# Performance work log

Hardware: AMD Instinct MI355X
Metric: run time of the kernel (lower is better)

## Reference

```python
import jax, jax.numpy as jnp
import numpy as np

N = 100000   # nodes
E = 1600000  # edges
R = 8        # relations
B = 8        # bases (min(R, hidden))
IN = 128; HID = 128; OUT = 128
BN_EPS = 1e-5


def setup_inputs() -> dict:
    key = jax.random.key(0)
    ks = jax.random.split(key, 20)
    s = 0.1  # xavier-ish small gain as in reset_parameters
    f32 = jnp.float32
    inp = {
        'x': jax.random.normal(ks[0], (N, IN), f32),
        'edge_index': jax.random.randint(ks[1], (2, E), 0, N, dtype=jnp.int32),
        'edge_type': jax.random.randint(ks[2], (E,), 0, R, dtype=jnp.int32),
        # RGCNConv layer 1 (basis decomposition)
        'basis1': jax.random.normal(ks[3], (B, IN, HID), f32) * s,
        'comp1': jax.random.normal(ks[4], (R, B), f32) * s,
        'root1': jax.random.normal(ks[5], (IN, HID), f32) * s,
        'bias1': jnp.zeros((HID,), f32),
        # layer 2
        'basis2': jax.random.normal(ks[6], (B, HID, HID), f32) * s,
        'comp2': jax.random.normal(ks[7], (R, B), f32) * s,
        'root2': jax.random.normal(ks[8], (HID, HID), f32) * s,
        'bias2': jnp.zeros((HID,), f32),
        # layer 3
        'basis3': jax.random.normal(ks[9], (B, HID, OUT), f32) * s,
        'comp3': jax.random.normal(ks[10], (R, B), f32) * s,
        'root3': jax.random.normal(ks[11], (HID, OUT), f32) * s,
        'bias3': jnp.zeros((OUT,), f32),
        # BatchNorm affine params (batch-stat normalization)
        'bn1_gamma': jnp.ones((HID,), f32),
        'bn1_beta': jnp.zeros((HID,), f32),
        'bn2_gamma': jnp.ones((HID,), f32),
        'bn2_beta': jnp.zeros((HID,), f32),
    }
    return inp


def rgcn_conv(x, basis, comp, root, bias, src, dst, etype):
    # relation weights from basis decomposition: W[r] = sum_b comp[r,b] * basis[b]
    W = jnp.einsum('rb,bio->rio', comp, basis)  # [R, in, out]
    # mean aggregation per (dst, relation); transform after mean (linearity)
    seg = dst.astype(jnp.int32) * R + etype.astype(jnp.int32)  # [E]
    msg_sum = jax.ops.segment_sum(x[src], seg, num_segments=N * R)  # [N*R, in]
    cnt = jax.ops.segment_sum(jnp.ones((src.shape[0],), x.dtype), seg, num_segments=N * R)
    mean = msg_sum / jnp.maximum(cnt, 1.0)[:, None]
    mean = mean.reshape(N, R, -1)  # [N, R, in]
    out = jnp.einsum('nri,rio->no', mean, W) + x @ root + bias
    return out


def batchnorm(h, gamma, beta):
    m = h.mean(axis=0)
    v = h.var(axis=0)
    return (h - m) * jax.lax.rsqrt(v + BN_EPS) * gamma + beta


def reference(x, edge_index, edge_type,
              basis1, comp1, root1, bias1,
              basis2, comp2, root2, bias2,
              basis3, comp3, root3, bias3,
              bn1_gamma, bn1_beta, bn2_gamma, bn2_beta):
    src, dst = edge_index[0], edge_index[1]
    h = rgcn_conv(x, basis1, comp1, root1, bias1, src, dst, edge_type)
    h = batchnorm(h, bn1_gamma, bn1_beta)
    h = jnp.where(h > 0, h, 0.1 * h)  # LeakyReLU(0.1); dropout inactive (eval)
    h = rgcn_conv(h, basis2, comp2, root2, bias2, src, dst, edge_type)
    h = batchnorm(h, bn2_gamma, bn2_beta)
    h = jnp.where(h > 0, h, 0.1 * h)
    h = rgcn_conv(h, basis3, comp3, root3, bias3, src, dst, edge_type)
    # F.normalize(p=2, dim=1)
    norm = jnp.maximum(jnp.sqrt(jnp.sum(h * h, axis=1, keepdims=True)), 1e-12)
    return h / norm
```

## Files before the change

### kernel.cpp

```cpp
#include <hip/hip_runtime.h>

#define NN 100000
#define EE 1600000
#define RRR 8
#define NSEG (NN*RRR)
#define F 128
#define KDIM 1152
#define NKT 36
#define BNEPS 1e-5f

typedef __attribute__((ext_vector_type(8))) short bf16x8;
typedef __attribute__((ext_vector_type(8))) unsigned short u16x8;
typedef __attribute__((ext_vector_type(4))) float f32x4;

static __device__ __forceinline__ unsigned short bf16r(float f) {
  unsigned u = __float_as_uint(f);
  u += 0x7fffu + ((u >> 16) & 1u);
  return (unsigned short)(u >> 16);
}
static __device__ __forceinline__ float b2f(unsigned short s) {
  return __uint_as_float((unsigned)s << 16);
}

__global__ void k_count(const int* __restrict__ dst, const int* __restrict__ et,
                        unsigned* __restrict__ cnt) {
  int e = blockIdx.x*256 + threadIdx.x;
  if (e < EE) {
    int seg = dst[e]*RRR + et[e];
    atomicAdd(&cnt[seg], 1u);
  }
}

__global__ void k_scan1(const unsigned* __restrict__ cnt, unsigned* __restrict__ off,
                        unsigned* __restrict__ bsum) {
  __shared__ unsigned s[256];
  int t = threadIdx.x;
  int base = blockIdx.x*2048 + t*8;
  unsigned loc[8];
  unsigned tot = 0;
#pragma unroll
  for (int j = 0; j < 8; j++) {
    unsigned v = (base+j < NSEG) ? cnt[base+j] : 0u;
    loc[j] = tot;
    tot += v;
  }
  s[t] = tot;
  __syncthreads();
  for (int d = 1; d < 256; d <<= 1) {
    unsigned v = (t >= d) ? s[t-d] : 0u;
    __syncthreads();
    s[t] += v;
    __syncthreads();
  }
  unsigned tbase = s[t] - tot;
#pragma unroll
  for (int j = 0; j < 8; j++)
    if (base+j < NSEG) off[base+j] = tbase + loc[j];
  if (t == 255) bsum[blockIdx.x] = s[255];
}

__global__ void k_scan2(unsigned* bsum, int nb) {
  __shared__ unsigned s[512];
  int t = threadIdx.x;
  unsigned v = (t < nb) ? bsum[t] : 0u;
  s[t] = v;
  __syncthreads();
  for (int d = 1; d < 512; d <<= 1) {
    unsigned u = (t >= d) ? s[t-d] : 0u;
    __syncthreads();
    s[t] += u;
    __syncthreads();
  }
  if (t < nb) bsum[t] = (t == 0) ? 0u : s[t-1];
}

__global__ void k_scan3(unsigned* off, const unsigned* __restrict__ bsum) {
  int i = blockIdx.x*256 + threadIdx.x;
  if (i < NSEG) off[i] += bsum[i >> 11];
}

__global__ void k_fill(const int* __restrict__ src, const int* __restrict__ dst,
                       const int* __restrict__ et, const unsigned* __restrict__ off,
                       unsigned* __restrict__ fillc, int* __restrict__ csr) {
  int e = blockIdx.x*256 + threadIdx.x;
  if (e < EE) {
    int seg = dst[e]*RRR + et[e];
    unsigned pos = off[seg] + atomicAdd(&fillc[seg], 1u);
    csr[pos] = src[e];
  }
}

__global__ void k_cvt(const float* __restrict__ x, unsigned short* __restrict__ xb) {
  int i = blockIdx.x*256 + threadIdx.x;
  if (i < NN*32) {
    float4 v = ((const float4*)x)[i];
    ushort4 o;
    o.x = bf16r(v.x); o.y = bf16r(v.y); o.z = bf16r(v.z); o.w = bf16r(v.w);
    ((ushort4*)xb)[i] = o;
  }
}

__global__ void k_makeW(const float* __restrict__ basis, const float* __restrict__ comp,
                        const float* __restrict__ root, unsigned short* __restrict__ WB) {
  int kt = blockIdx.x;
  int ct = blockIdx.y;
  int lane = threadIdx.x;
  int o = ct*16 + (lane & 15);
  int kbase = kt*32 + (lane >> 4)*8;
  unsigned short v[8];
#pragma unroll
  for (int j = 0; j < 8; j++) {
    int k = kbase + j;
    float val;
    if (k < 1024) {
      int r = k >> 7, i = k & 127;
      val = 0.f;
#pragma unroll
      for (int b = 0; b < 8; b++)
        val += comp[r*8+b] * basis[(b*F + i)*F + o];
    } else {
      val = root[(k - 1024)*F + o];
    }
    v[j] = bf16r(val);
  }
  unsigned short* dst = WB + ((size_t)(kt*8 + ct)*64 + lane)*8;
#pragma unroll
  for (int j = 0; j < 8; j++) dst[j] = v[j];
}

__global__ __launch_bounds__(256) void k_agg(const unsigned short* __restrict__ hb,
    const unsigned* __restrict__ off, const unsigned* __restrict__ cnt,
    const int* __restrict__ csr, unsigned short* __restrict__ Mean,
    int base, int count) {
  int t = threadIdx.x;
  int sl = t & 15;
  int c8 = sl * 8;
  int sidx = t >> 4;
  int nl = sidx >> 3;
  int r  = sidx & 7;
  int nloc = blockIdx.x*2 + nl;
  if (nloc > count-1) nloc = count-1;
  int node = base + nloc;
  int seg = node*RRR + r;
  unsigned b0 = off[seg];
  unsigned k = cnt[seg];
  float a[8];
#pragma unroll
  for (int u = 0; u < 8; u++) a[u] = 0.f;
  unsigned j = 0;
  for (; j + 2 <= k; j += 2) {
    int iA = csr[b0+j];
    int iB = csr[b0+j+1];
    u16x8 va = *(const u16x8*)&hb[(size_t)iA*F + c8];
    u16x8 vb = *(const u16x8*)&hb[(size_t)iB*F + c8];
#pragma unroll
    for (int u = 0; u < 8; u++) a[u] += b2f(va[u]) + b2f(vb[u]);
  }
  if (j < k) {
    int iA = csr[b0+j];
    u16x8 va = *(const u16x8*)&hb[(size_t)iA*F + c8];
#pragma unroll
    for (int u = 0; u < 8; u++) a[u] += b2f(va[u]);
  }
  float inv = k ? 1.f/(float)k : 0.f;
  u16x8 o;
#pragma unroll
  for (int u = 0; u < 8; u++) o[u] = bf16r(a[u]*inv);
  size_t mrow = (size_t)nloc * KDIM;
  *(u16x8*)&Mean[mrow + r*F + c8] = o;
  if (r == 0)
    *(u16x8*)&Mean[mrow + 1024 + c8] = *(const u16x8*)&hb[(size_t)node*F + c8];
}

__global__ __launch_bounds__(256) void k_gemm(const unsigned short* __restrict__ Mean,
    const unsigned short* __restrict__ WB, const float* __restrict__ bias,
    float* __restrict__ outp, float* __restrict__ stats,
    int outBase, int count, int mode) {
  __shared__ float s_sum[128];
  __shared__ float s_sq[128];
  int t = threadIdx.x;
  int wave = t >> 6;
  int lane = t & 63;
  int rbase = blockIdx.x*128 + wave*32;
  int rlo = lane & 15;
  int kg = lane >> 4;
  int r0 = rbase + rlo;       if (r0 > count-1) r0 = count-1;
  int r1 = rbase + 16 + rlo;  if (r1 > count-1) r1 = count-1;
  const unsigned short* a0p = Mean + (size_t)r0*KDIM + kg*8;
  const unsigned short* a1p = Mean + (size_t)r1*KDIM + kg*8;
  const unsigned short* bp  = WB + (size_t)lane*8;

  if (mode == 0 && t < 128) { s_sum[t] = 0.f; s_sq[t] = 0.f; }

  f32x4 acc[2][8];
#pragma unroll
  for (int i = 0; i < 2; i++)
#pragma unroll
    for (int j = 0; j < 8; j++) acc[i][j] = (f32x4){0.f,0.f,0.f,0.f};

  for (int kt = 0; kt < NKT; kt++) {
    bf16x8 a0 = *(const bf16x8*)(a0p + kt*32);
    bf16x8 a1 = *(const bf16x8*)(a1p + kt*32);
#pragma unroll
    for (int ct = 0; ct < 8; ct++) {
      bf16x8 b = *(const bf16x8*)(bp + (size_t)(kt*8 + ct)*64*8);
      acc[0][ct] = __builtin_amdgcn_mfma_f32_16x16x32_bf16(a0, b, acc[0][ct], 0, 0, 0);
      acc[1][ct] = __builtin_amdgcn_mfma_f32_16x16x32_bf16(a1, b, acc[1][ct], 0, 0, 0);
    }
  }

  float bv[8];
#pragma unroll
  for (int ct = 0; ct < 8; ct++) bv[ct] = bias[ct*16 + rlo];

  if (mode == 0) {
    __syncthreads();
    float psum[8], psq[8];
#pragma unroll
    for (int ct = 0; ct < 8; ct++) { psum[ct] = 0.f; psq[ct] = 0.f; }
#pragma unroll
    for (int rt = 0; rt < 2; rt++) {
#pragma unroll
      for (int i = 0; i < 4; i++) {
        int row = rbase + rt*16 + kg*4 + i;
        if (row < count) {
          float* orow = outp + (size_t)(outBase + row)*F;
#pragma unroll
          for (int ct = 0; ct < 8; ct++) {
            float y = acc[rt][ct][i] + bv[ct];
            orow[ct*16 + rlo] = y;
            psum[ct] += y;
            psq[ct]  += y*y;
          }
        }
      }
    }
#pragma unroll
    for (int ct = 0; ct < 8; ct++) {
      atomicAdd(&s_sum[ct*16 + rlo], psum[ct]);
      atomicAdd(&s_sq [ct*16 + rlo], psq[ct]);
    }
    __syncthreads();
    if (t < 128) {
      atomicAdd(&stats[t],       s_sum[t]);
      atomicAdd(&stats[128 + t], s_sq[t]);
    }
  } else {
#pragma unroll
    for (int rt = 0; rt < 2; rt++) {
#pragma unroll
      for (int i = 0; i < 4; i++) {
        int row = rbase + rt*16 + kg*4 + i;
        float y[8];
        float ss = 0.f;
#pragma unroll
        for (int ct = 0; ct < 8; ct++) {
          y[ct] = acc[rt][ct][i] + bv[ct];
          ss += y[ct]*y[ct];
        }
#pragma unroll
        for (int m = 1; m < 16; m <<= 1)
          ss += __shfl_xor(ss, m, 64);
        float inv = 1.f / fmaxf(sqrtf(ss), 1e-12f);
        if (row < count) {
          float* orow = outp + (size_t)(outBase + row)*F;
#pragma unroll
          for (int ct = 0; ct < 8; ct++)
            orow[ct*16 + rlo] = y[ct]*inv;
        }
      }
    }
  }
}

__global__ __launch_bounds__(256) void k_bnapply(const float* __restrict__ h,
    const float* __restrict__ stats, const float* __restrict__ gamma,
    const float* __restrict__ beta, unsigned short* __restrict__ outp) {
  int idx = blockIdx.x*256 + threadIdx.x;
  if (idx >= NN*32) return;
  int row = idx >> 5;
  int c4 = (idx & 31) * 4;
  float4 v  = *(const float4*)&h[(size_t)row*F + c4];
  float4 sm = *(const float4*)&stats[c4];
  float4 sq = *(const float4*)&stats[128 + c4];
  float4 g  = *(const float4*)&gamma[c4];
  float4 bt = *(const float4*)&beta[c4];
  const float invN = 1.f / (float)NN;
  ushort4 o;
  { float m = sm.x*invN; float var = sq.x*invN - m*m; float r0 = rsqrtf(var + BNEPS);
    float z = (v.x - m)*r0*g.x + bt.x; o.x = bf16r((z > 0.f) ? z : 0.1f*z); }
  { float m = sm.y*invN; float var = sq.y*invN - m*m; float r0 = rsqrtf(var + BNEPS);
    float z = (v.y - m)*r0*g.y + bt.y; o.y = bf16r((z > 0.f) ? z : 0.1f*z); }
  { float m = sm.z*invN; float var = sq.z*invN - m*m; float r0 = rsqrtf(var + BNEPS);
    float z = (v.z - m)*r0*g.z + bt.z; o.z = bf16r((z > 0.f) ? z : 0.1f*z); }
  { float m = sm.w*invN; float var = sq.w*invN - m*m; float r0 = rsqrtf(var + BNEPS);
    float z = (v.w - m)*r0*g.w + bt.w; o.w = bf16r((z > 0.f) ? z : 0.1f*z); }
  *(ushort4*)&outp[(size_t)row*F + c4] = o;
}

extern "C" void kernel_launch(void* const* d_in, const int* in_sizes, int n_in,
                              void* d_out, int out_size, void* d_ws, size_t ws_size,
                              hipStream_t stream) {
  const float* x      = (const float*)d_in[0];
  const int*   ei     = (const int*)d_in[1];
  const int*   etp    = (const int*)d_in[2];
  const float* basis[3] = {(const float*)d_in[3], (const float*)d_in[7],  (const float*)d_in[11]};
  const float* comp[3]  = {(const float*)d_in[4], (const float*)d_in[8],  (const float*)d_in[12]};
  const float* root[3]  = {(const float*)d_in[5], (const float*)d_in[9],  (const float*)d_in[13]};
  const float* bias[3]  = {(const float*)d_in[6], (const float*)d_in[10], (const float*)d_in[14]};
  const float* gamma[2] = {(const float*)d_in[15], (const float*)d_in[17]};
  const float* beta[2]  = {(const float*)d_in[16], (const float*)d_in[18]};
  const int* srcv = ei;
  const int* dstv = ei + EE;
  float* out = (float*)d_out;

  char* w = (char*)d_ws;
  size_t p = 0;
  auto take = [&](size_t bytes) -> void* {
    void* q = w + p;
    p = (p + bytes + 255) & ~(size_t)255;
    return q;
  };
  unsigned* cnt   = (unsigned*)take((size_t)NSEG*4);
  unsigned* off   = (unsigned*)take((size_t)NSEG*4);
  unsigned* fillc = (unsigned*)take((size_t)NSEG*4);
  int*      csr   = (int*)     take((size_t)EE*4);
  unsigned* bsum  = (unsigned*)take(1024*4);
  unsigned short* WB = (unsigned short*)take((size_t)KDIM*F*2);
  float*    stats = (float*)   take(256*4);
  float*    wsA   = (float*)   take((size_t)NN*F*4);
  unsigned short* wsBb = (unsigned short*)take((size_t)NN*F*2);
  unsigned short* xb   = (unsigned short*)take((size_t)NN*F*2);
  size_t avail = (ws_size > p) ? (ws_size - p) : 0;
  long long chmax = (long long)(avail / ((size_t)KDIM*2));
  int CH = (chmax > NN) ? NN : (int)chmax;
  if (CH < 2) CH = 2;
  unsigned short* Mean = (unsigned short*)(w + p);

  hipMemsetAsync(cnt,   0, (size_t)NSEG*4, stream);
  hipMemsetAsync(fillc, 0, (size_t)NSEG*4, stream);
  k_count<<<(EE+255)/256, 256, 0, stream>>>(dstv, etp, cnt);
  int nb1 = (NSEG + 2047)/2048;
  k_scan1<<<nb1, 256, 0, stream>>>(cnt, off, bsum);
  k_scan2<<<1, 512, 0, stream>>>(bsum, nb1);
  k_scan3<<<(NSEG+255)/256, 256, 0, stream>>>(off, bsum);
  k_fill<<<(EE+255)/256, 256, 0, stream>>>(srcv, dstv, etp, off, fillc, csr);
  k_cvt<<<(NN*32+255)/256, 256, 0, stream>>>(x, xb);

  for (int l = 0; l < 3; l++) {
    const unsigned short* hin = (l == 0) ? xb : wsBb;
    float* hraw = (l == 2) ? out : wsA;
    int mode = (l == 2) ? 1 : 0;
    dim3 gw(NKT, 8);
    k_makeW<<<gw, 64, 0, stream>>>(basis[l], comp[l], root[l], WB);
    if (l < 2) hipMemsetAsync(stats, 0, 256*4, stream);
    for (int b0n = 0; b0n < NN; b0n += CH) {
      int cc = NN - b0n; if (cc > CH) cc = CH;
      k_agg<<<(cc+1)/2, 256, 0, stream>>>(hin, off, cnt, csr, Mean, b0n, cc);
      k_gemm<<<(cc+127)/128, 256, 0, stream>>>(Mean, WB, bias[l], hraw, stats, b0n, cc, mode);
    }
    if (l < 2)
      k_bnapply<<<(NN*32+255)/256, 256, 0, stream>>>(hraw, stats, gamma[l], beta[l], wsBb);
  }
}
```

Baseline: 897.9 us.

## Fuse aggregation into GEMM via LDS tiles and rebuild CSR with bucketed sort

The per-layer aggregation and GEMM kernels become one fused kernel. It builds each relation's mean (and the root slice) for 64 nodes into swizzled LDS, then feeds MFMA directly, so the large bf16 Mean buffer in global memory is no longer written and re-read. The CSR build is also replaced by a two-level bucket sort: a coarse histogram and scatter by destination block, then per-bucket local counting in LDS. This avoids global atomics over 800K segments and the multi-pass scan. In exchange, aggregation work is serialized per relation behind barriers inside each block, which can reduce latency hiding, and src is packed into 17 bits.

```diff
diff --git a/kernel.cpp b/kernel.cpp
--- a/kernel.cpp
+++ b/kernel.cpp
@@ -5,8 +5,8 @@
 #define RRR 8
 #define NSEG (NN*RRR)
 #define F 128
-#define KDIM 1152
-#define NKT 36
+#define NBK 196
+#define NT 64
 #define BNEPS 1e-5f
 
 typedef __attribute__((ext_vector_type(8))) short bf16x8;
@@ -21,72 +21,90 @@
 static __device__ __forceinline__ float b2f(unsigned short s) {
   return __uint_as_float((unsigned)s << 16);
 }
-
-__global__ void k_count(const int* __restrict__ dst, const int* __restrict__ et,
-                        unsigned* __restrict__ cnt) {
+static __device__ __forceinline__ int swz(int a) {
+  return a ^ (((a >> 8) & 7) << 4);
+}
+
+__global__ void k_hist(const int* __restrict__ dst, unsigned* __restrict__ bhist) {
+  __shared__ unsigned h[NBK];
+  int t = threadIdx.x;
+  if (t < NBK) h[t] = 0;
+  __syncthreads();
+  for (int e = blockIdx.x*256 + t; e < EE; e += gridDim.x*256)
+    atomicAdd(&h[((unsigned)dst[e]) >> 9], 1u);
+  __syncthreads();
+  if (t < NBK) atomicAdd(&bhist[t], h[t]);
+}
+
+__global__ void k_scanb(const unsigned* __restrict__ bhist, unsigned* __restrict__ boff) {
+  __shared__ unsigned s[256];
+  int t = threadIdx.x;
+  unsigned v = (t < NBK) ? bhist[t] : 0u;
+  s[t] = v;
+  __syncthreads();
+  for (int d = 1; d < 256; d <<= 1) {
+    unsigned u = (t >= d) ? s[t-d] : 0u;
+    __syncthreads();
+    s[t] += u;
+    __syncthreads();
+  }
+  if (t < NBK) boff[t] = s[t] - v;
+  if (t == NBK-1) boff[NBK] = s[t];
+}
+
+__global__ void k_scatter(const int* __restrict__ src, const int* __restrict__ dst,
+                          const int* __restrict__ et, const unsigned* __restrict__ boff,
+                          unsigned* __restrict__ bfill, unsigned* __restrict__ ebuf) {
   int e = blockIdx.x*256 + threadIdx.x;
   if (e < EE) {
-    int seg = dst[e]*RRR + et[e];
-    atomicAdd(&cnt[seg], 1u);
-  }
-}
-
-__global__ void k_scan1(const unsigned* __restrict__ cnt, unsigned* __restrict__ off,
-                        unsigned* __restrict__ bsum) {
-  __shared__ unsigned s[256];
-  int t = threadIdx.x;
-  int base = blockIdx.x*2048 + t*8;
-  unsigned loc[8];
-  unsigned tot = 0;
-#pragma unroll
-  for (int j = 0; j < 8; j++) {
-    unsigned v = (base+j < NSEG) ? cnt[base+j] : 0u;
-    loc[j] = tot;
-    tot += v;
-  }
-  s[t] = tot;
+    int d = dst[e];
+    int b = ((unsigned)d) >> 9;
+    unsigned pos = boff[b] + atomicAdd(&bfill[b], 1u);
+    ebuf[pos] = (((unsigned)((d & 511)*RRR + et[e])) << 17) | (unsigned)src[e];
+  }
+}
+
+__global__ __launch_bounds__(256) void k_bucket(const unsigned* __restrict__ boff,
+    const unsigned* __restrict__ ebuf, unsigned* __restrict__ off,
+    unsigned* __restrict__ cnt, int* __restrict__ csr) {
+  __shared__ unsigned lcnt[4096];
+  __shared__ unsigned loff[4096];
+  __shared__ unsigned wsum[256];
+  int b = blockIdx.x, t = threadIdx.x;
+  unsigned s0 = boff[b], e0 = boff[b+1];
+  for (int i = t; i < 4096; i += 256) lcnt[i] = 0;
+  __syncthreads();
+  for (unsigned i = s0 + t; i < e0; i += 256)
+    atomicAdd(&lcnt[ebuf[i] >> 17], 1u);
+  __syncthreads();
+  unsigned run = 0, tmp[16];
+  int base16 = t*16;
+#pragma unroll
+  for (int j = 0; j < 16; j++) { tmp[j] = run; run += lcnt[base16 + j]; }
+  wsum[t] = run;
   __syncthreads();
   for (int d = 1; d < 256; d <<= 1) {
-    unsigned v = (t >= d) ? s[t-d] : 0u;
-    __syncthreads();
-    s[t] += v;
-    __syncthreads();
-  }
-  unsigned tbase = s[t] - tot;
-#pragma unroll
-  for (int j = 0; j < 8; j++)
-    if (base+j < NSEG) off[base+j] = tbase + loc[j];
-  if (t == 255) bsum[blockIdx.x] = s[255];
-}
-
-__global__ void k_scan2(unsigned* bsum, int nb) {
-  __shared__ unsigned s[512];
-  int t = threadIdx.x;
-  unsigned v = (t < nb) ? bsum[t] : 0u;
-  s[t] = v;
-  __syncthreads();
-  for (int d = 1; d < 512; d <<= 1) {
-    unsigned u = (t >= d) ? s[t-d] : 0u;
-    __syncthreads();
-    s[t] += u;
-    __syncthreads();
-  }
-  if (t < nb) bsum[t] = (t == 0) ? 0u : s[t-1];
-}
-
-__global__ void k_scan3(unsigned* off, const unsigned* __restrict__ bsum) {
-  int i = blockIdx.x*256 + threadIdx.x;
-  if (i < NSEG) off[i] += bsum[i >> 11];
-}
-
-__global__ void k_fill(const int* __restrict__ src, const int* __restrict__ dst,
-                       const int* __restrict__ et, const unsigned* __restrict__ off,
-                       unsigned* __restrict__ fillc, int* __restrict__ csr) {
-  int e = blockIdx.x*256 + threadIdx.x;
-  if (e < EE) {
-    int seg = dst[e]*RRR + et[e];
-    unsigned pos = off[seg] + atomicAdd(&fillc[seg], 1u);
-    csr[pos] = src[e];
+    unsigned u = (t >= d) ? wsum[t-d] : 0u;
+    __syncthreads();
+    wsum[t] += u;
+    __syncthreads();
+  }
+  unsigned tb = wsum[t] - run;
+#pragma unroll
+  for (int j = 0; j < 16; j++) loff[base16 + j] = tb + tmp[j];
+  __syncthreads();
+  int gbase = b*4096;
+  for (int i = t; i < 4096; i += 256) {
+    int gseg = gbase + i;
+    if (gseg < NSEG) { off[gseg] = s0 + loff[i]; cnt[gseg] = lcnt[i]; }
+  }
+  for (int i = t; i < 4096; i += 256) lcnt[i] = 0;
+  __syncthreads();
+  for (unsigned i = s0 + t; i < e0; i += 256) {
+    unsigned p = ebuf[i];
+    unsigned ls = p >> 17;
+    unsigned r = atomicAdd(&lcnt[ls], 1u);
+    csr[s0 + loff[ls] + r] = (int)(p & 0x1FFFFu);
   }
 }
 
@@ -116,96 +134,83 @@
       int r = k >> 7, i = k & 127;
       val = 0.f;
 #pragma unroll
-      for (int b = 0; b < 8; b++)
-        val += comp[r*8+b] * basis[(b*F + i)*F + o];
+      for (int bb = 0; bb < 8; bb++)
+        val += comp[r*8+bb] * basis[(bb*F + i)*F + o];
     } else {
       val = root[(k - 1024)*F + o];
     }
     v[j] = bf16r(val);
   }
-  unsigned short* dst = WB + ((size_t)(kt*8 + ct)*64 + lane)*8;
-#pragma unroll
-  for (int j = 0; j < 8; j++) dst[j] = v[j];
-}
-
-__global__ __launch_bounds__(256) void k_agg(const unsigned short* __restrict__ hb,
+  unsigned short* dstp = WB + ((size_t)(kt*8 + ct)*64 + lane)*8;
+#pragma unroll
+  for (int j = 0; j < 8; j++) dstp[j] = v[j];
+}
+
+__global__ __launch_bounds__(256) void k_fused(const unsigned short* __restrict__ hb,
     const unsigned* __restrict__ off, const unsigned* __restrict__ cnt,
-    const int* __restrict__ csr, unsigned short* __restrict__ Mean,
-    int base, int count) {
+    const int* __restrict__ csr, const unsigned short* __restrict__ WB,
+    const float* __restrict__ bias, float* __restrict__ outp,
+    float* __restrict__ stats, int mode) {
+  __shared__ __align__(16) char lds[NT*256];
+  __shared__ float s_sum[128], s_sq[128];
   int t = threadIdx.x;
-  int sl = t & 15;
-  int c8 = sl * 8;
-  int sidx = t >> 4;
-  int nl = sidx >> 3;
-  int r  = sidx & 7;
-  int nloc = blockIdx.x*2 + nl;
-  if (nloc > count-1) nloc = count-1;
-  int node = base + nloc;
-  int seg = node*RRR + r;
-  unsigned b0 = off[seg];
-  unsigned k = cnt[seg];
-  float a[8];
-#pragma unroll
-  for (int u = 0; u < 8; u++) a[u] = 0.f;
-  unsigned j = 0;
-  for (; j + 2 <= k; j += 2) {
-    int iA = csr[b0+j];
-    int iB = csr[b0+j+1];
-    u16x8 va = *(const u16x8*)&hb[(size_t)iA*F + c8];
-    u16x8 vb = *(const u16x8*)&hb[(size_t)iB*F + c8];
-#pragma unroll
-    for (int u = 0; u < 8; u++) a[u] += b2f(va[u]) + b2f(vb[u]);
-  }
-  if (j < k) {
-    int iA = csr[b0+j];
-    u16x8 va = *(const u16x8*)&hb[(size_t)iA*F + c8];
-#pragma unroll
-    for (int u = 0; u < 8; u++) a[u] += b2f(va[u]);
-  }
-  float inv = k ? 1.f/(float)k : 0.f;
-  u16x8 o;
-#pragma unroll
-  for (int u = 0; u < 8; u++) o[u] = bf16r(a[u]*inv);
-  size_t mrow = (size_t)nloc * KDIM;
-  *(u16x8*)&Mean[mrow + r*F + c8] = o;
-  if (r == 0)
-    *(u16x8*)&Mean[mrow + 1024 + c8] = *(const u16x8*)&hb[(size_t)node*F + c8];
-}
-
-__global__ __launch_bounds__(256) void k_gemm(const unsigned short* __restrict__ Mean,
-    const unsigned short* __restrict__ WB, const float* __restrict__ bias,
-    float* __restrict__ outp, float* __restrict__ stats,
-    int outBase, int count, int mode) {
-  __shared__ float s_sum[128];
-  __shared__ float s_sq[128];
-  int t = threadIdx.x;
-  int wave = t >> 6;
-  int lane = t & 63;
-  int rbase = blockIdx.x*128 + wave*32;
-  int rlo = lane & 15;
-  int kg = lane >> 4;
-  int r0 = rbase + rlo;       if (r0 > count-1) r0 = count-1;
-  int r1 = rbase + 16 + rlo;  if (r1 > count-1) r1 = count-1;
-  const unsigned short* a0p = Mean + (size_t)r0*KDIM + kg*8;
-  const unsigned short* a1p = Mean + (size_t)r1*KDIM + kg*8;
-  const unsigned short* bp  = WB + (size_t)lane*8;
-
+  int lane = t & 63, wave = t >> 6;
+  int g = t >> 4, sl = t & 15;
+  int rlo = lane & 15, kg = lane >> 4;
+  int n0 = blockIdx.x * NT;
   if (mode == 0 && t < 128) { s_sum[t] = 0.f; s_sq[t] = 0.f; }
 
-  f32x4 acc[2][8];
-#pragma unroll
-  for (int i = 0; i < 2; i++)
-#pragma unroll
-    for (int j = 0; j < 8; j++) acc[i][j] = (f32x4){0.f,0.f,0.f,0.f};
-
-  for (int kt = 0; kt < NKT; kt++) {
-    bf16x8 a0 = *(const bf16x8*)(a0p + kt*32);
-    bf16x8 a1 = *(const bf16x8*)(a1p + kt*32);
-#pragma unroll
-    for (int ct = 0; ct < 8; ct++) {
-      bf16x8 b = *(const bf16x8*)(bp + (size_t)(kt*8 + ct)*64*8);
-      acc[0][ct] = __builtin_amdgcn_mfma_f32_16x16x32_bf16(a0, b, acc[0][ct], 0, 0, 0);
-      acc[1][ct] = __builtin_amdgcn_mfma_f32_16x16x32_bf16(a1, b, acc[1][ct], 0, 0, 0);
+  f32x4 acc[8];
+#pragma unroll
+  for (int j = 0; j < 8; j++) acc[j] = (f32x4){0.f, 0.f, 0.f, 0.f};
+
+  for (int c = 0; c < 9; c++) {
+    __syncthreads();
+#pragma unroll
+    for (int nn = 0; nn < 4; nn++) {
+      int row = g*4 + nn;
+      int node = n0 + row;
+      int nodec = (node < NN) ? node : NN-1;
+      u16x8 o;
+      if (c < 8) {
+        int seg = nodec*RRR + c;
+        unsigned b0 = off[seg], k = cnt[seg];
+        float a[8];
+#pragma unroll
+        for (int u = 0; u < 8; u++) a[u] = 0.f;
+        unsigned j = 0;
+        for (; j + 2 <= k; j += 2) {
+          int iA = csr[b0+j];
+          int iB = csr[b0+j+1];
+          u16x8 va = *(const u16x8*)&hb[(size_t)iA*F + sl*8];
+          u16x8 vb = *(const u16x8*)&hb[(size_t)iB*F + sl*8];
+#pragma unroll
+          for (int u = 0; u < 8; u++) a[u] += b2f(va[u]) + b2f(vb[u]);
+        }
+        if (j < k) {
+          int iA = csr[b0+j];
+          u16x8 va = *(const u16x8*)&hb[(size_t)iA*F + sl*8];
+#pragma unroll
+          for (int u = 0; u < 8; u++) a[u] += b2f(va[u]);
+        }
+        float inv = k ? 1.f/(float)k : 0.f;
+#pragma unroll
+        for (int u = 0; u < 8; u++) o[u] = bf16r(a[u]*inv);
+      } else {
+        o = *(const u16x8*)&hb[(size_t)nodec*F + sl*8];
+      }
+      *(u16x8*)(lds + swz(row*256 + sl*16)) = o;
+    }
+    __syncthreads();
+#pragma unroll
+    for (int kt = 0; kt < 4; kt++) {
+      bf16x8 a = *(const bf16x8*)(lds + swz((wave*16 + rlo)*256 + kt*64 + kg*16));
+      const unsigned short* bp = WB + ((size_t)((c*4 + kt)*8)*64 + lane)*8;
+#pragma unroll
+      for (int ct = 0; ct < 8; ct++) {
+        bf16x8 bfr = *(const bf16x8*)(bp + (size_t)ct*64*8);
+        acc[ct] = __builtin_amdgcn_mfma_f32_16x16x32_bf16(a, bfr, acc[ct], 0, 0, 0);
+      }
     }
   }
 
@@ -214,24 +219,20 @@
   for (int ct = 0; ct < 8; ct++) bv[ct] = bias[ct*16 + rlo];
 
   if (mode == 0) {
-    __syncthreads();
     float psum[8], psq[8];
 #pragma unroll
     for (int ct = 0; ct < 8; ct++) { psum[ct] = 0.f; psq[ct] = 0.f; }
 #pragma unroll
-    for (int rt = 0; rt < 2; rt++) {
-#pragma unroll
-      for (int i = 0; i < 4; i++) {
-        int row = rbase + rt*16 + kg*4 + i;
-        if (row < count) {
-          float* orow = outp + (size_t)(outBase + row)*F;
-#pragma unroll
-          for (int ct = 0; ct < 8; ct++) {
-            float y = acc[rt][ct][i] + bv[ct];
-            orow[ct*16 + rlo] = y;
-            psum[ct] += y;
-            psq[ct]  += y*y;
-          }
+    for (int i = 0; i < 4; i++) {
+      int row = n0 + wave*16 + kg*4 + i;
+      if (row < NN) {
+        float* orow = outp + (size_t)row*F;
+#pragma unroll
+        for (int ct = 0; ct < 8; ct++) {
+          float y = acc[ct][i] + bv[ct];
+          orow[ct*16 + rlo] = y;
+          psum[ct] += y;
+          psq[ct]  += y*y;
         }
       }
     }
@@ -247,27 +248,23 @@
     }
   } else {
 #pragma unroll
-    for (int rt = 0; rt < 2; rt++) {
-#pragma unroll
-      for (int i = 0; i < 4; i++) {
-        int row = rbase + rt*16 + kg*4 + i;
-        float y[8];
-        float ss = 0.f;
-#pragma unroll
-        for (int ct = 0; ct < 8; ct++) {
-          y[ct] = acc[rt][ct][i] + bv[ct];
-          ss += y[ct]*y[ct];
-        }
-#pragma unroll
-        for (int m = 1; m < 16; m <<= 1)
-          ss += __shfl_xor(ss, m, 64);
-        float inv = 1.f / fmaxf(sqrtf(ss), 1e-12f);
-        if (row < count) {
-          float* orow = outp + (size_t)(outBase + row)*F;
-#pragma unroll
-          for (int ct = 0; ct < 8; ct++)
-            orow[ct*16 + rlo] = y[ct]*inv;
-        }
+    for (int i = 0; i < 4; i++) {
+      int row = n0 + wave*16 + kg*4 + i;
+      float y[8], ss = 0.f;
+#pragma unroll
+      for (int ct = 0; ct < 8; ct++) {
+        y[ct] = acc[ct][i] + bv[ct];
+        ss += y[ct]*y[ct];
+      }
+#pragma unroll
+      for (int m = 1; m < 16; m <<= 1)
+        ss += __shfl_xor(ss, m, 64);
+      float inv = 1.f / fmaxf(sqrtf(ss), 1e-12f);
+      if (row < NN) {
+        float* orow = outp + (size_t)row*F;
+#pragma unroll
+        for (int ct = 0; ct < 8; ct++)
+          orow[ct*16 + rlo] = y[ct]*inv;
       }
     }
   }
@@ -283,18 +280,18 @@
   float4 v  = *(const float4*)&h[(size_t)row*F + c4];
   float4 sm = *(const float4*)&stats[c4];
   float4 sq = *(const float4*)&stats[128 + c4];
-  float4 g  = *(const float4*)&gamma[c4];
+  float4 gm = *(const float4*)&gamma[c4];
   float4 bt = *(const float4*)&beta[c4];
   const float invN = 1.f / (float)NN;
   ushort4 o;
   { float m = sm.x*invN; float var = sq.x*invN - m*m; float r0 = rsqrtf(var + BNEPS);
-    float z = (v.x - m)*r0*g.x + bt.x; o.x = bf16r((z > 0.f) ? z : 0.1f*z); }
+    float z = (v.x - m)*r0*gm.x + bt.x; o.x = bf16r((z > 0.f) ? z : 0.1f*z); }
   { float m = sm.y*invN; float var = sq.y*invN - m*m; float r0 = rsqrtf(var + BNEPS);
-    float z = (v.y - m)*r0*g.y + bt.y; o.y = bf16r((z > 0.f) ? z : 0.1f*z); }
+    float z = (v.y - m)*r0*gm.y + bt.y; o.y = bf16r((z > 0.f) ? z : 0.1f*z); }
   { float m = sm.z*invN; float var = sq.z*invN - m*m; float r0 = rsqrtf(var + BNEPS);
-    float z = (v.z - m)*r0*g.z + bt.z; o.z = bf16r((z > 0.f) ? z : 0.1f*z); }
+    float z = (v.z - m)*r0*gm.z + bt.z; o.z = bf16r((z > 0.f) ? z : 0.1f*z); }
   { float m = sm.w*invN; float var = sq.w*invN - m*m; float r0 = rsqrtf(var + BNEPS);
-    float z = (v.w - m)*r0*g.w + bt.w; o.w = bf16r((z > 0.f) ? z : 0.1f*z); }
+    float z = (v.w - m)*r0*gm.w + bt.w; o.w = bf16r((z > 0.f) ? z : 0.1f*z); }
   *(ushort4*)&outp[(size_t)row*F + c4] = o;
 }
 
@@ -323,42 +320,35 @@
   };
   unsigned* cnt   = (unsigned*)take((size_t)NSEG*4);
   unsigned* off   = (unsigned*)take((size_t)NSEG*4);
-  unsigned* fillc = (unsigned*)take((size_t)NSEG*4);
   int*      csr   = (int*)     take((size_t)EE*4);
-  unsigned* bsum  = (unsigned*)take(1024*4);
-  unsigned short* WB = (unsigned short*)take((size_t)KDIM*F*2);
+  unsigned* ebuf  = (unsigned*)take((size_t)EE*4);
+  unsigned* bhist = (unsigned*)take((size_t)NBK*4);
+  unsigned* boff  = (unsigned*)take((size_t)(NBK+1)*4);
+  unsigned* bfill = (unsigned*)take((size_t)NBK*4);
+  unsigned short* WB = (unsigned short*)take((size_t)1152*F*2);
   float*    stats = (float*)   take(256*4);
   float*    wsA   = (float*)   take((size_t)NN*F*4);
   unsigned short* wsBb = (unsigned short*)take((size_t)NN*F*2);
   unsigned short* xb   = (unsigned short*)take((size_t)NN*F*2);
-  size_t avail = (ws_size > p) ? (ws_size - p) : 0;
-  long long chmax = (long long)(avail / ((size_t)KDIM*2));
-  int CH = (chmax > NN) ? NN : (int)chmax;
-  if (CH < 2) CH = 2;
-  unsigned short* Mean = (unsigned short*)(w + p);
-
-  hipMemsetAsync(cnt,   0, (size_t)NSEG*4, stream);
-  hipMemsetAsync(fillc, 0, (size_t)NSEG*4, stream);
-  k_count<<<(EE+255)/256, 256, 0, stream>>>(dstv, etp, cnt);
-  int nb1 = (NSEG + 2047)/2048;
-  k_scan1<<<nb1, 256, 0, stream>>>(cnt, off, bsum);
-  k_scan2<<<1, 512, 0, stream>>>(bsum, nb1);
-  k_scan3<<<(NSEG+255)/256, 256, 0, stream>>>(off, bsum);
-  k_fill<<<(EE+255)/256, 256, 0, stream>>>(srcv, dstv, etp, off, fillc, csr);
+  (void)ws_size;
+
+  hipMemsetAsync(bhist, 0, (size_t)NBK*4, stream);
+  hipMemsetAsync(bfill, 0, (size_t)NBK*4, stream);
+  k_hist<<<256, 256, 0, stream>>>(dstv, bhist);
+  k_scanb<<<1, 256, 0, stream>>>(bhist, boff);
+  k_scatter<<<(EE+255)/256, 256, 0, stream>>>(srcv, dstv, etp, boff, bfill, ebuf);
+  k_bucket<<<NBK, 256, 0, stream>>>(boff, ebuf, off, cnt, csr);
   k_cvt<<<(NN*32+255)/256, 256, 0, stream>>>(x, xb);
 
+  int NB = (NN + NT - 1) / NT;
   for (int l = 0; l < 3; l++) {
     const unsigned short* hin = (l == 0) ? xb : wsBb;
     float* hraw = (l == 2) ? out : wsA;
     int mode = (l == 2) ? 1 : 0;
-    dim3 gw(NKT, 8);
+    dim3 gw(36, 8);
     k_makeW<<<gw, 64, 0, stream>>>(basis[l], comp[l], root[l], WB);
     if (l < 2) hipMemsetAsync(stats, 0, 256*4, stream);
-    for (int b0n = 0; b0n < NN; b0n += CH) {
-      int cc = NN - b0n; if (cc > CH) cc = CH;
-      k_agg<<<(cc+1)/2, 256, 0, stream>>>(hin, off, cnt, csr, Mean, b0n, cc);
-      k_gemm<<<(cc+127)/128, 256, 0, stream>>>(Mean, WB, bias[l], hraw, stats, b0n, cc, mode);
-    }
+    k_fused<<<NB, 256, 0, stream>>>(hin, off, cnt, csr, WB, bias[l], hraw, stats, mode);
     if (l < 2)
       k_bnapply<<<(NN*32+255)/256, 256, 0, stream>>>(hraw, stats, gamma[l], beta[l], wsBb);
   }
```

After: 1.865 ms. 108% more time.

## Fuse setup kernels, precompute all layer weights, drop self-row copy in aggregation

Applied to the files above, without the earlier changes.

Merges the x-to-bf16 conversion with edge counting, drops the separate fill counter by atomically bumping the offsets in place, and builds all three layers' weight matrices in one launch that also zeroes the BN stats. The aggregation kernel now processes two contiguous segments per thread group and stops copying the self row into the Mean buffer; the GEMM reads the root-input rows straight from the hidden-state buffer instead. This cuts launches, memsets and Mean-buffer traffic. It adds interleaved dual-segment loop control, and the chunk size is now rounded down to a multiple of 4.

```diff
diff --git a/kernel.cpp b/kernel.cpp
--- a/kernel.cpp
+++ b/kernel.cpp
@@ -5,8 +5,6 @@
 #define RRR 8
 #define NSEG (NN*RRR)
 #define F 128
-#define KDIM 1152
-#define NKT 36
 #define BNEPS 1e-5f
 
 typedef __attribute__((ext_vector_type(8))) short bf16x8;
@@ -22,13 +20,18 @@
   return __uint_as_float((unsigned)s << 16);
 }
 
-__global__ void k_count(const int* __restrict__ dst, const int* __restrict__ et,
-                        unsigned* __restrict__ cnt) {
-  int e = blockIdx.x*256 + threadIdx.x;
-  if (e < EE) {
-    int seg = dst[e]*RRR + et[e];
-    atomicAdd(&cnt[seg], 1u);
-  }
+__global__ __launch_bounds__(256) void k_precnt(const float* __restrict__ x,
+    unsigned short* __restrict__ xb, const int* __restrict__ dst,
+    const int* __restrict__ et, unsigned* __restrict__ cnt) {
+  int idx = blockIdx.x*256 + threadIdx.x;
+  if (idx < NN*32) {
+    float4 v = ((const float4*)x)[idx];
+    ushort4 o;
+    o.x = bf16r(v.x); o.y = bf16r(v.y); o.z = bf16r(v.z); o.w = bf16r(v.w);
+    ((ushort4*)xb)[idx] = o;
+  }
+  if (idx < EE)
+    atomicAdd(&cnt[dst[idx]*RRR + et[idx]], 1u);
 }
 
 __global__ void k_scan1(const unsigned* __restrict__ cnt, unsigned* __restrict__ off,
@@ -80,31 +83,31 @@
 }
 
 __global__ void k_fill(const int* __restrict__ src, const int* __restrict__ dst,
-                       const int* __restrict__ et, const unsigned* __restrict__ off,
-                       unsigned* __restrict__ fillc, int* __restrict__ csr) {
+                       const int* __restrict__ et, unsigned* __restrict__ off,
+                       int* __restrict__ csr) {
   int e = blockIdx.x*256 + threadIdx.x;
   if (e < EE) {
     int seg = dst[e]*RRR + et[e];
-    unsigned pos = off[seg] + atomicAdd(&fillc[seg], 1u);
+    unsigned pos = atomicAdd(&off[seg], 1u);
     csr[pos] = src[e];
   }
 }
 
-__global__ void k_cvt(const float* __restrict__ x, unsigned short* __restrict__ xb) {
-  int i = blockIdx.x*256 + threadIdx.x;
-  if (i < NN*32) {
-    float4 v = ((const float4*)x)[i];
-    ushort4 o;
-    o.x = bf16r(v.x); o.y = bf16r(v.y); o.z = bf16r(v.z); o.w = bf16r(v.w);
-    ((ushort4*)xb)[i] = o;
-  }
-}
-
-__global__ void k_makeW(const float* __restrict__ basis, const float* __restrict__ comp,
-                        const float* __restrict__ root, unsigned short* __restrict__ WB) {
-  int kt = blockIdx.x;
-  int ct = blockIdx.y;
+__global__ void k_makeW3(const float* __restrict__ b1, const float* __restrict__ c1,
+                         const float* __restrict__ r1, const float* __restrict__ b2,
+                         const float* __restrict__ c2, const float* __restrict__ r2,
+                         const float* __restrict__ b3, const float* __restrict__ c3,
+                         const float* __restrict__ r3, unsigned short* __restrict__ WB3,
+                         float* __restrict__ stats) {
+  int kt = blockIdx.x, ct = blockIdx.y, l = blockIdx.z;
   int lane = threadIdx.x;
+  if (kt == 0 && ct == 0 && l == 0) {
+#pragma unroll
+    for (int j = 0; j < 8; j++) stats[lane*8 + j] = 0.f;
+  }
+  const float* basis = (l == 0) ? b1 : (l == 1) ? b2 : b3;
+  const float* comp  = (l == 0) ? c1 : (l == 1) ? c2 : c3;
+  const float* root  = (l == 0) ? r1 : (l == 1) ? r2 : r3;
   int o = ct*16 + (lane & 15);
   int kbase = kt*32 + (lane >> 4)*8;
   unsigned short v[8];
@@ -116,66 +119,76 @@
       int r = k >> 7, i = k & 127;
       val = 0.f;
 #pragma unroll
-      for (int b = 0; b < 8; b++)
-        val += comp[r*8+b] * basis[(b*F + i)*F + o];
+      for (int bb = 0; bb < 8; bb++)
+        val += comp[r*8+bb] * basis[(bb*F + i)*F + o];
     } else {
       val = root[(k - 1024)*F + o];
     }
     v[j] = bf16r(val);
   }
-  unsigned short* dst = WB + ((size_t)(kt*8 + ct)*64 + lane)*8;
-#pragma unroll
-  for (int j = 0; j < 8; j++) dst[j] = v[j];
+  unsigned short* dstp = WB3 + (size_t)l*1152*F + ((size_t)(kt*8 + ct)*64 + lane)*8;
+#pragma unroll
+  for (int j = 0; j < 8; j++) dstp[j] = v[j];
 }
 
 __global__ __launch_bounds__(256) void k_agg(const unsigned short* __restrict__ hb,
     const unsigned* __restrict__ off, const unsigned* __restrict__ cnt,
-    const int* __restrict__ csr, unsigned short* __restrict__ Mean,
-    int base, int count) {
+    const int* __restrict__ csr, unsigned short* __restrict__ Mean, int segBase) {
   int t = threadIdx.x;
-  int sl = t & 15;
-  int c8 = sl * 8;
-  int sidx = t >> 4;
-  int nl = sidx >> 3;
-  int r  = sidx & 7;
-  int nloc = blockIdx.x*2 + nl;
-  if (nloc > count-1) nloc = count-1;
-  int node = base + nloc;
-  int seg = node*RRR + r;
-  unsigned b0 = off[seg];
-  unsigned k = cnt[seg];
-  float a[8];
-#pragma unroll
-  for (int u = 0; u < 8; u++) a[u] = 0.f;
-  unsigned j = 0;
-  for (; j + 2 <= k; j += 2) {
-    int iA = csr[b0+j];
-    int iB = csr[b0+j+1];
-    u16x8 va = *(const u16x8*)&hb[(size_t)iA*F + c8];
-    u16x8 vb = *(const u16x8*)&hb[(size_t)iB*F + c8];
-#pragma unroll
-    for (int u = 0; u < 8; u++) a[u] += b2f(va[u]) + b2f(vb[u]);
-  }
-  if (j < k) {
-    int iA = csr[b0+j];
-    u16x8 va = *(const u16x8*)&hb[(size_t)iA*F + c8];
-#pragma unroll
-    for (int u = 0; u < 8; u++) a[u] += b2f(va[u]);
-  }
-  float inv = k ? 1.f/(float)k : 0.f;
-  u16x8 o;
-#pragma unroll
-  for (int u = 0; u < 8; u++) o[u] = bf16r(a[u]*inv);
-  size_t mrow = (size_t)nloc * KDIM;
-  *(u16x8*)&Mean[mrow + r*F + c8] = o;
-  if (r == 0)
-    *(u16x8*)&Mean[mrow + 1024 + c8] = *(const u16x8*)&hb[(size_t)node*F + c8];
+  int sl = t & 15, c8 = sl*8;
+  int g = t >> 4;
+  int s0 = segBase + blockIdx.x*32 + 2*g;
+  int s1 = s0 + 1;
+  unsigned cA = cnt[s0], cB = cnt[s1];
+  unsigned bA = off[s0] - cA, bB = off[s1] - cB;
+  const unsigned short* hc = hb + c8;
+  float aA[8], aB[8];
+#pragma unroll
+  for (int u = 0; u < 8; u++) { aA[u] = 0.f; aB[u] = 0.f; }
+  unsigned jA = 0, jB = 0;
+  while (jA < cA || jB < cB) {
+    unsigned nA = cA - jA; if (nA > 2) nA = 2;
+    unsigned nB = cB - jB; if (nB > 2) nB = 2;
+    int i0 = 0, i1 = 0, i2 = 0, i3 = 0;
+    if (nA > 0) i0 = csr[bA + jA];
+    if (nA > 1) i1 = csr[bA + jA + 1];
+    if (nB > 0) i2 = csr[bB + jB];
+    if (nB > 1) i3 = csr[bB + jB + 1];
+    if (nA > 0) {
+      u16x8 v = *(const u16x8*)&hc[(size_t)i0*F];
+#pragma unroll
+      for (int u = 0; u < 8; u++) aA[u] += b2f(v[u]);
+    }
+    if (nA > 1) {
+      u16x8 v = *(const u16x8*)&hc[(size_t)i1*F];
+#pragma unroll
+      for (int u = 0; u < 8; u++) aA[u] += b2f(v[u]);
+    }
+    if (nB > 0) {
+      u16x8 v = *(const u16x8*)&hc[(size_t)i2*F];
+#pragma unroll
+      for (int u = 0; u < 8; u++) aB[u] += b2f(v[u]);
+    }
+    if (nB > 1) {
+      u16x8 v = *(const u16x8*)&hc[(size_t)i3*F];
+#pragma unroll
+      for (int u = 0; u < 8; u++) aB[u] += b2f(v[u]);
+    }
+    jA += nA; jB += nB;
+  }
+  float ivA = cA ? 1.f/(float)cA : 0.f;
+  float ivB = cB ? 1.f/(float)cB : 0.f;
+  u16x8 oA, oB;
+#pragma unroll
+  for (int u = 0; u < 8; u++) { oA[u] = bf16r(aA[u]*ivA); oB[u] = bf16r(aB[u]*ivB); }
+  *(u16x8*)&Mean[(size_t)(s0 - segBase)*F + c8] = oA;
+  *(u16x8*)&Mean[(size_t)(s1 - segBase)*F + c8] = oB;
 }
 
 __global__ __launch_bounds__(256) void k_gemm(const unsigned short* __restrict__ Mean,
-    const unsigned short* __restrict__ WB, const float* __restrict__ bias,
-    float* __restrict__ outp, float* __restrict__ stats,
-    int outBase, int count, int mode) {
+    const unsigned short* __restrict__ hb, const unsigned short* __restrict__ WB,
+    const float* __restrict__ bias, float* __restrict__ outp,
+    float* __restrict__ stats, int outBase, int count, int mode) {
   __shared__ float s_sum[128];
   __shared__ float s_sq[128];
   int t = threadIdx.x;
@@ -186,8 +199,10 @@
   int kg = lane >> 4;
   int r0 = rbase + rlo;       if (r0 > count-1) r0 = count-1;
   int r1 = rbase + 16 + rlo;  if (r1 > count-1) r1 = count-1;
-  const unsigned short* a0p = Mean + (size_t)r0*KDIM + kg*8;
-  const unsigned short* a1p = Mean + (size_t)r1*KDIM + kg*8;
+  const unsigned short* a0p = Mean + (size_t)r0*1024 + kg*8;
+  const unsigned short* a1p = Mean + (size_t)r1*1024 + kg*8;
+  const unsigned short* s0p = hb + (size_t)(outBase + r0)*F + kg*8;
+  const unsigned short* s1p = hb + (size_t)(outBase + r1)*F + kg*8;
   const unsigned short* bp  = WB + (size_t)lane*8;
 
   if (mode == 0 && t < 128) { s_sum[t] = 0.f; s_sq[t] = 0.f; }
@@ -198,9 +213,21 @@
 #pragma unroll
     for (int j = 0; j < 8; j++) acc[i][j] = (f32x4){0.f,0.f,0.f,0.f};
 
-  for (int kt = 0; kt < NKT; kt++) {
+#pragma unroll 4
+  for (int kt = 0; kt < 32; kt++) {
     bf16x8 a0 = *(const bf16x8*)(a0p + kt*32);
     bf16x8 a1 = *(const bf16x8*)(a1p + kt*32);
+#pragma unroll
+    for (int ct = 0; ct < 8; ct++) {
+      bf16x8 b = *(const bf16x8*)(bp + (size_t)(kt*8 + ct)*64*8);
+      acc[0][ct] = __builtin_amdgcn_mfma_f32_16x16x32_bf16(a0, b, acc[0][ct], 0, 0, 0);
+      acc[1][ct] = __builtin_amdgcn_mfma_f32_16x16x32_bf16(a1, b, acc[1][ct], 0, 0, 0);
+    }
+  }
+#pragma unroll
+  for (int kt = 32; kt < 36; kt++) {
+    bf16x8 a0 = *(const bf16x8*)(s0p + (kt-32)*32);
+    bf16x8 a1 = *(const bf16x8*)(s1p + (kt-32)*32);
 #pragma unroll
     for (int ct = 0; ct < 8; ct++) {
       bf16x8 b = *(const bf16x8*)(bp + (size_t)(kt*8 + ct)*64*8);
@@ -251,8 +278,7 @@
 #pragma unroll
       for (int i = 0; i < 4; i++) {
         int row = rbase + rt*16 + kg*4 + i;
-        float y[8];
-        float ss = 0.f;
+        float y[8], ss = 0.f;
 #pragma unroll
         for (int ct = 0; ct < 8; ct++) {
           y[ct] = acc[rt][ct][i] + bv[ct];
@@ -283,18 +309,18 @@
   float4 v  = *(const float4*)&h[(size_t)row*F + c4];
   float4 sm = *(const float4*)&stats[c4];
   float4 sq = *(const float4*)&stats[128 + c4];
-  float4 g  = *(const float4*)&gamma[c4];
+  float4 gm = *(const float4*)&gamma[c4];
   float4 bt = *(const float4*)&beta[c4];
   const float invN = 1.f / (float)NN;
   ushort4 o;
   { float m = sm.x*invN; float var = sq.x*invN - m*m; float r0 = rsqrtf(var + BNEPS);
-    float z = (v.x - m)*r0*g.x + bt.x; o.x = bf16r((z > 0.f) ? z : 0.1f*z); }
+    float z = (v.x - m)*r0*gm.x + bt.x; o.x = bf16r((z > 0.f) ? z : 0.1f*z); }
   { float m = sm.y*invN; float var = sq.y*invN - m*m; float r0 = rsqrtf(var + BNEPS);
-    float z = (v.y - m)*r0*g.y + bt.y; o.y = bf16r((z > 0.f) ? z : 0.1f*z); }
+    float z = (v.y - m)*r0*gm.y + bt.y; o.y = bf16r((z > 0.f) ? z : 0.1f*z); }
   { float m = sm.z*invN; float var = sq.z*invN - m*m; float r0 = rsqrtf(var + BNEPS);
-    float z = (v.z - m)*r0*g.z + bt.z; o.z = bf16r((z > 0.f) ? z : 0.1f*z); }
+    float z = (v.z - m)*r0*gm.z + bt.z; o.z = bf16r((z > 0.f) ? z : 0.1f*z); }
   { float m = sm.w*invN; float var = sq.w*invN - m*m; float r0 = rsqrtf(var + BNEPS);
-    float z = (v.w - m)*r0*g.w + bt.w; o.w = bf16r((z > 0.f) ? z : 0.1f*z); }
+    float z = (v.w - m)*r0*gm.w + bt.w; o.w = bf16r((z > 0.f) ? z : 0.1f*z); }
   *(ushort4*)&outp[(size_t)row*F + c4] = o;
 }
 
@@ -323,43 +349,43 @@
   };
   unsigned* cnt   = (unsigned*)take((size_t)NSEG*4);
   unsigned* off   = (unsigned*)take((size_t)NSEG*4);
-  unsigned* fillc = (unsigned*)take((size_t)NSEG*4);
   int*      csr   = (int*)     take((size_t)EE*4);
   unsigned* bsum  = (unsigned*)take(1024*4);
-  unsigned short* WB = (unsigned short*)take((size_t)KDIM*F*2);
-  float*    stats = (float*)   take(256*4);
+  unsigned short* WB3 = (unsigned short*)take((size_t)3*1152*F*2);
+  float*    stats = (float*)   take(512*4);
   float*    wsA   = (float*)   take((size_t)NN*F*4);
   unsigned short* wsBb = (unsigned short*)take((size_t)NN*F*2);
   unsigned short* xb   = (unsigned short*)take((size_t)NN*F*2);
   size_t avail = (ws_size > p) ? (ws_size - p) : 0;
-  long long chmax = (long long)(avail / ((size_t)KDIM*2));
-  int CH = (chmax > NN) ? NN : (int)chmax;
-  if (CH < 2) CH = 2;
+  long long chmax = (long long)(avail / (1024*2));
+  int CH = (chmax > NN) ? NN : (int)(chmax & ~3LL);
+  if (CH < 4) CH = 4;
   unsigned short* Mean = (unsigned short*)(w + p);
 
-  hipMemsetAsync(cnt,   0, (size_t)NSEG*4, stream);
-  hipMemsetAsync(fillc, 0, (size_t)NSEG*4, stream);
-  k_count<<<(EE+255)/256, 256, 0, stream>>>(dstv, etp, cnt);
+  hipMemsetAsync(cnt, 0, (size_t)NSEG*4, stream);
+  k_precnt<<<12500, 256, 0, stream>>>(x, xb, dstv, etp, cnt);
   int nb1 = (NSEG + 2047)/2048;
   k_scan1<<<nb1, 256, 0, stream>>>(cnt, off, bsum);
   k_scan2<<<1, 512, 0, stream>>>(bsum, nb1);
   k_scan3<<<(NSEG+255)/256, 256, 0, stream>>>(off, bsum);
-  k_fill<<<(EE+255)/256, 256, 0, stream>>>(srcv, dstv, etp, off, fillc, csr);
-  k_cvt<<<(NN*32+255)/256, 256, 0, stream>>>(x, xb);
+  k_fill<<<(EE+255)/256, 256, 0, stream>>>(srcv, dstv, etp, off, csr);
+  dim3 gw(36, 8, 3);
+  k_makeW3<<<gw, 64, 0, stream>>>(basis[0], comp[0], root[0],
+                                  basis[1], comp[1], root[1],
+                                  basis[2], comp[2], root[2], WB3, stats);
 
   for (int l = 0; l < 3; l++) {
     const unsigned short* hin = (l == 0) ? xb : wsBb;
     float* hraw = (l == 2) ? out : wsA;
     int mode = (l == 2) ? 1 : 0;
-    dim3 gw(NKT, 8);
-    k_makeW<<<gw, 64, 0, stream>>>(basis[l], comp[l], root[l], WB);
-    if (l < 2) hipMemsetAsync(stats, 0, 256*4, stream);
+    const unsigned short* WB = WB3 + (size_t)l*1152*F;
+    float* st = stats + (size_t)(l == 2 ? 0 : l)*256;
     for (int b0n = 0; b0n < NN; b0n += CH) {
       int cc = NN - b0n; if (cc > CH) cc = CH;
-      k_agg<<<(cc+1)/2, 256, 0, stream>>>(hin, off, cnt, csr, Mean, b0n, cc);
-      k_gemm<<<(cc+127)/128, 256, 0, stream>>>(Mean, WB, bias[l], hraw, stats, b0n, cc, mode);
+      k_agg<<<cc*8/32, 256, 0, stream>>>(hin, off, cnt, csr, Mean, b0n*8);
+      k_gemm<<<(cc+127)/128, 256, 0, stream>>>(Mean, hin, WB, bias[l], hraw, st, b0n, cc, mode);
     }
     if (l < 2)
-      k_bnapply<<<(NN*32+255)/256, 256, 0, stream>>>(hraw, stats, gamma[l], beta[l], wsBb);
-  }
-}
+      k_bnapply<<<12500, 256, 0, stream>>>(hraw, stats + (size_t)l*256, gamma[l], beta[l], wsBb);
+  }
+}
```

After: 1.319 ms. 46.9% more time.
